# Kernel tuning notes

Measured on AMD Instinct MI355X. Metric: run time of the kernel, lower is better.

The kernel has to match this reference:

```python
import jax, jax.numpy as jnp
import numpy as np

B, L, D, NH = 4, 1500, 512, 8
HD = D // NH
EPS = 1e-8            # F.normalize eps
PEPS = 1.1920929e-07  # torch clamp_probs eps for float32
TEMP = 1.0


def setup_inputs():
    key = jax.random.key(0)
    ks = jax.random.split(key, 12)
    s = 1.0 / np.sqrt(D)
    eye = jnp.eye(D, dtype=jnp.float32)
    return {
        "hidden": jax.random.normal(ks[0], (B, L, D), jnp.float32),
        "lengths": jnp.ones((B,), jnp.float32),
        "u_noise": jax.random.uniform(ks[1], (B, L), jnp.float32),
        "W1": jax.random.normal(ks[2], (D, D), jnp.float32) * s,
        "b1": jnp.zeros((D,), jnp.float32),
        "W2": jax.random.normal(ks[3], (D, D), jnp.float32) * s,
        "b2": jnp.zeros((D,), jnp.float32),
        "Wq": eye + jax.random.normal(ks[4], (D, D), jnp.float32) * 0.01,
        "Wk": eye + jax.random.normal(ks[5], (D, D), jnp.float32) * 0.01,
        "sim_bias": jnp.float32(0.098),
        "learned_query": jax.random.normal(ks[6], (D,), jnp.float32),
        "Wpk": eye + jax.random.normal(ks[7], (D, D), jnp.float32) * 0.01,
        "Wpv": eye + jax.random.normal(ks[8], (D, D), jnp.float32) * 0.01,
        "Wpo": eye + jax.random.normal(ks[9], (D, D), jnp.float32) * 0.01,
        "ln_g": jnp.ones((D,), jnp.float32),
        "ln_b": jnp.zeros((D,), jnp.float32),
    }


def reference(hidden, lengths, u_noise, W1, b1, W2, b2, Wq, Wk, sim_bias,
              learned_query, Wpk, Wpv, Wpo, ln_g, ln_b):
    Bb, Ll, Dd = hidden.shape

    def nrm(x):
        n = jnp.sqrt(jnp.sum(x * x, -1, keepdims=True))
        return x / jnp.maximum(n, EPS)

    def mlp(x):
        return jax.nn.gelu(x @ W1.T + b1, approximate=False) @ W2.T + b2

    # boundary logits from adjacent-frame cosine similarity (dropout = eval identity)
    q_in = nrm(hidden[:, :-1]); q = nrm(mlp(q_in) + q_in) @ Wq.T
    k_in = nrm(hidden[:, 1:]);  k = nrm(mlp(k_in) + k_in) @ Wk.T
    cos = jnp.sum(q * k, -1)                                   # (B, L-1)
    probs = jnp.clip((1.0 - (cos + sim_bias)) * 0.5, 0.0, 1.0)
    probs = jnp.pad(probs, ((0, 0), (0, 1)))                   # (B, L)

    # RelaxedBernoulli rsample with explicit logistic noise
    p = jnp.clip(probs, PEPS, 1.0 - PEPS)
    u = jnp.clip(u_noise, PEPS, 1.0 - PEPS)
    soft = jax.nn.sigmoid((jnp.log(p) - jnp.log1p(-p) + jnp.log(u) - jnp.log1p(-u)) / TEMP)
    hard = (soft > 0.5).astype(hidden.dtype)

    idx = jnp.arange(Ll)
    valid_len = jnp.minimum((lengths * (Ll + 1)).astype(jnp.int32) - 1, Ll)
    trunc = (valid_len < Ll)[:, None]
    zmask = trunc & (idx[None] >= valid_len[:, None])
    omask = trunc & (idx[None] == valid_len[:, None])
    soft = jnp.where(omask, 1.0, jnp.where(zmask, 0.0, soft))
    hard = jnp.where(omask, 1.0, jnp.where(zmask, 0.0, hard))
    hard_b = hard - jax.lax.stop_gradient(soft) + soft         # straight-through
    # emergency boundary for all-zero rows
    no_b = (jnp.sum(hard, 1) == 0)[:, None]
    hard_b = jnp.where(no_b & (idx[None] == jnp.minimum(valid_len, Ll - 1)[:, None]), 1.0, hard_b)

    # segment membership (common()): token l in segment s iff exclusive cumsum == s
    seg = jnp.cumsum(hard_b, 1) - hard_b                       # (B, L)
    lmask = idx[None] < (lengths * Ll).astype(jnp.int32)[:, None]
    seg_mask = (seg[:, :, None] == idx[None, None, :].astype(hidden.dtype)) & lmask[:, :, None]  # (B,L,S)

    # layernorm + K/V projections
    mu = jnp.mean(hidden, -1, keepdims=True)
    hv = hidden - mu
    hn = hv / jnp.sqrt(jnp.mean(hv * hv, -1, keepdims=True) + 1e-5) * ln_g + ln_b
    keys = (hn @ Wpk.T).reshape(Bb, Ll, NH, HD)
    vals = (hn @ Wpv.T).reshape(Bb, Ll, NH, HD)

    # query is shared across segments -> scores only differ via the segment mask
    qh = learned_query.reshape(NH, HD)
    base = jnp.einsum('hd,blhd->bhl', qh, keys) * (HD ** -0.5)  # (B,H,L)
    mask_t = jnp.transpose(seg_mask, (0, 2, 1))[:, None]        # (B,1,S,L)
    sc = jnp.where(mask_t, base[:, :, None, :], -jnp.inf)       # (B,H,S,L)
    aw = jnp.nan_to_num(jax.nn.softmax(sc, axis=-1))            # empty segments -> 0 rows
    pooled = jnp.einsum('bhsl,blhd->bshd', aw, vals).reshape(Bb, Ll, Dd)
    return pooled @ Wpo.T                                       # (B, S=L, D)
```

## Files before the change

### kernel.cpp

```cpp
#include <hip/hip_runtime.h>
#include <math.h>

#define Bz 4
#define Lz 1500
#define Dz 512
#define NHz 8
#define Nz (Bz*Lz)
#define PEPSf 1.1920929e-07f

typedef __bf16 bf16x8 __attribute__((ext_vector_type(8)));
typedef unsigned short u16x8 __attribute__((ext_vector_type(8)));
typedef float f32x4 __attribute__((ext_vector_type(4)));
typedef unsigned short us;

__device__ __forceinline__ us f2bf(float f) {
  unsigned u = __float_as_uint(f);
  return (us)((u + 0x7fffu + ((u >> 16) & 1u)) >> 16);
}
__device__ __forceinline__ float bf2f(us b) {
  return __uint_as_float(((unsigned)b) << 16);
}
__device__ __forceinline__ int ti_idx(int row, int col) {
  return (((row >> 4) * 64 + (col >> 3)) << 7) + ((row & 15) << 3) + (col & 7);
}
__device__ __forceinline__ void st_tiled(us* __restrict__ P, int row, int col, us v) {
  P[ti_idx(row, col)] = v;
}

__device__ __forceinline__ bool decode_blk(int bx, int ncg, int& R, int& cg) {
  int xcd = bx & 7, v = bx >> 3;
  cg = v % ncg;
  R = (v / ncg) * 8 + xcd;
  return R < 94;
}

__global__ __launch_bounds__(256) void k_wconv(
    const float* __restrict__ s0, const float* __restrict__ s1, const float* __restrict__ s2,
    const float* __restrict__ s3,
    const float* __restrict__ Wq, const float* __restrict__ Wk,
    const float* __restrict__ Wpk, const float* __restrict__ lq,
    us* __restrict__ h0, us* __restrict__ h1, us* __restrict__ h2, us* __restrict__ h3,
    us* __restrict__ l0, us* __restrict__ l1,
    us* __restrict__ WkTh, us* __restrict__ WkTl, us* __restrict__ WqTh, us* __restrict__ WqTl,
    float* __restrict__ wqe) {
  const int rt = blockIdx.x, mat = blockIdx.y, t = threadIdx.x;
  if (mat == 8) {
    if (rt < 8) {
      for (int d = t; d < Dz; d += 256) {
        float acc = 0.f;
        for (int e = 0; e < 64; ++e) acc += lq[rt * 64 + e] * Wpk[(size_t)(rt * 64 + e) * Dz + d];
        wqe[rt * Dz + d] = acc;
      }
    }
    return;
  }
  const float* S; us* H; us* L = nullptr; bool tr = false;
  switch (mat) {
    case 0: S = s0; H = h0; L = l0; break;
    case 1: S = s1; H = h1; L = l1; break;
    case 2: S = s2; H = h2; break;
    case 3: S = s3; H = h3; break;
    case 4: S = Wk; H = WkTh; L = WkTl; tr = true; break;
    default: S = Wq; H = WqTh; L = WqTl; tr = true; break;
  }
  for (int e = t; e < 8192; e += 256) {
    int mm = e >> 9, c = e & 511;
    float x = tr ? S[(size_t)c * 512 + (rt * 16 + mm)]
                 : S[(size_t)(rt * 16 + mm) * 512 + c];
    us hb = f2bf(x);
    int off = ((rt * 64 + (c >> 3)) << 7) + (mm << 3) + (c & 7);
    H[off] = hb;
    if (L) L[off] = f2bf(x - bf2f(hb));
  }
}

__global__ __launch_bounds__(256) void k_rowprep(const float* __restrict__ h,
    const float* __restrict__ g, const float* __restrict__ bb,
    const float* __restrict__ wqe,
    us* __restrict__ Uh, us* __restrict__ Ul, us* __restrict__ HNh,
    float* __restrict__ base) {
  const int row = blockIdx.x;
  const int t = threadIdx.x;
  const float* x = h + (size_t)row * Dz;
  float x0 = x[t], x1 = x[t + 256];
  float s = x0 + x1, q = x0 * x0 + x1 * x1;
  #pragma unroll
  for (int o = 32; o > 0; o >>= 1) { s += __shfl_xor(s, o, 64); q += __shfl_xor(q, o, 64); }
  __shared__ float ls[4], lq[4];
  __shared__ float xs[Dz];
  if ((t & 63) == 0) { ls[t >> 6] = s; lq[t >> 6] = q; }
  __syncthreads();
  s = ls[0] + ls[1] + ls[2] + ls[3];
  q = lq[0] + lq[1] + lq[2] + lq[3];
  float un = 1.f / fmaxf(sqrtf(q), 1e-8f);
  float u0 = x0 * un, u1 = x1 * un;
  us hb0 = f2bf(u0), hb1 = f2bf(u1);
  st_tiled(Uh, row, t, hb0);       st_tiled(Ul, row, t, f2bf(u0 - bf2f(hb0)));
  st_tiled(Uh, row, t + 256, hb1); st_tiled(Ul, row, t + 256, f2bf(u1 - bf2f(hb1)));
  float mu = s * (1.f / 512.f);
  float var = fmaxf(q * (1.f / 512.f) - mu * mu, 0.f);
  float r = rsqrtf(var + 1e-5f);
  float hn0 = (x0 - mu) * r * g[t] + bb[t];
  float hn1 = (x1 - mu) * r * g[t + 256] + bb[t + 256];
  st_tiled(HNh, row, t, f2bf(hn0));
  st_tiled(HNh, row, t + 256, f2bf(hn1));
  xs[t] = hn0; xs[t + 256] = hn1;
  __syncthreads();
  const int hh = t >> 5, lane = t & 31;
  float accb = 0.f;
  for (int d = lane; d < Dz; d += 32) accb += xs[d] * wqe[hh * Dz + d];
  #pragma unroll
  for (int o = 16; o > 0; o >>= 1) accb += __shfl_xor(accb, o, 32);
  if (lane == 0) base[(size_t)row * NHz + hh] = accb * 0.125f;
}

template<int SPLIT>
__device__ __forceinline__ void gemm_body(
    const us* __restrict__ Ah, const us* __restrict__ Al,
    const us* __restrict__ Bh, const us* __restrict__ Bl,
    const float* __restrict__ bias,
    const us* __restrict__ addH, const us* __restrict__ addL, int doGelu,
    float* __restrict__ outF, us* __restrict__ outR,
    us* __restrict__ outH, us* __restrict__ outL,
    int R, int cg, int colbase, int Nrows) {
  const int t = threadIdx.x, w = t >> 6, l = t & 63;
  const int m = l & 15, q = l >> 4;
  const int wr = w & 1, wc = w >> 1;
  const int laneoff = q * 128 + m * 8;
  const int nrtm1 = (Nrows >> 4) - 1;

  const u16x8* pa[2]; const u16x8* pal[2];
  const u16x8* pb[2]; const u16x8* pbl[2];
  #pragma unroll
  for (int i = 0; i < 2; ++i) {
    int rt = min(R * 4 + wr * 2 + i, nrtm1);
    pa[i] = (const u16x8*)(Ah + (size_t)rt * 8192 + laneoff);
    if (SPLIT == 3) pal[i] = (const u16x8*)(Al + (size_t)rt * 8192 + laneoff);
  }
  #pragma unroll
  for (int j = 0; j < 2; ++j) {
    int ct = cg * 4 + wc * 2 + j;
    pb[j] = (const u16x8*)(Bh + (size_t)ct * 8192 + laneoff);
    if (SPLIT == 3) pbl[j] = (const u16x8*)(Bl + (size_t)ct * 8192 + laneoff);
  }

  u16x8 bAh[2][2], bAl[2][2], bBh[2][2], bBl[2][2];
  #pragma unroll
  for (int i = 0; i < 2; ++i) {
    bAh[0][i] = pa[i][0];
    if (SPLIT == 3) bAl[0][i] = pal[i][0];
  }
  #pragma unroll
  for (int j = 0; j < 2; ++j) {
    bBh[0][j] = pb[j][0];
    if (SPLIT == 3) bBl[0][j] = pbl[j][0];
  }

  f32x4 acc[2][2];
  #pragma unroll
  for (int i = 0; i < 2; ++i)
    #pragma unroll
    for (int j = 0; j < 2; ++j) acc[i][j] = (f32x4){0.f, 0.f, 0.f, 0.f};

  #pragma unroll 2
  for (int s = 0; s < 16; ++s) {
    const int cur = s & 1, nxt = cur ^ 1;
    const int sn = (s + 1) & 15;
    #pragma unroll
    for (int i = 0; i < 2; ++i) {
      bAh[nxt][i] = pa[i][sn * 64];
      if (SPLIT == 3) bAl[nxt][i] = pal[i][sn * 64];
    }
    #pragma unroll
    for (int j = 0; j < 2; ++j) {
      bBh[nxt][j] = pb[j][sn * 64];
      if (SPLIT == 3) bBl[nxt][j] = pbl[j][sn * 64];
    }
    #pragma unroll
    for (int i = 0; i < 2; ++i)
      #pragma unroll
      for (int j = 0; j < 2; ++j) {
        bf16x8 a = __builtin_bit_cast(bf16x8, bAh[cur][i]);
        bf16x8 b = __builtin_bit_cast(bf16x8, bBh[cur][j]);
        acc[i][j] = __builtin_amdgcn_mfma_f32_16x16x32_bf16(a, b, acc[i][j], 0, 0, 0);
        if (SPLIT == 3) {
          bf16x8 al_ = __builtin_bit_cast(bf16x8, bAl[cur][i]);
          bf16x8 bl_ = __builtin_bit_cast(bf16x8, bBl[cur][j]);
          acc[i][j] = __builtin_amdgcn_mfma_f32_16x16x32_bf16(a, bl_, acc[i][j], 0, 0, 0);
          acc[i][j] = __builtin_amdgcn_mfma_f32_16x16x32_bf16(al_, b, acc[i][j], 0, 0, 0);
        }
      }
  }

  const int row0 = R * 64 + wr * 32;
  const int col0 = colbase + wc * 32;
  #pragma unroll
  for (int i = 0; i < 2; ++i) {
    #pragma unroll
    for (int r = 0; r < 4; ++r) {
      const int grow = row0 + i * 16 + q * 4 + r;
      if (grow >= Nrows) continue;
      #pragma unroll
      for (int j = 0; j < 2; ++j) {
        const int gcol = col0 + j * 16 + m;
        float v = acc[i][j][r];
        if (bias)   v += bias[gcol];
        if (addH) {
          int ai = ti_idx(grow, gcol);
          v += bf2f(addH[ai]) + bf2f(addL[ai]);
        }
        if (doGelu) v = 0.5f * v * (1.f + erff(v * 0.70710678118654752f));
        if (outF) outF[(size_t)grow * Dz + gcol] = v;
        if (outR) outR[(size_t)grow * Dz + gcol] = f2bf(v);
        if (outH) {
          us hb = f2bf(v);
          st_tiled(outH, grow, gcol, hb);
          if (outL) st_tiled(outL, grow, gcol, f2bf(v - bf2f(hb)));
        }
      }
    }
  }
}

__global__ __launch_bounds__(256, 4) void g_t1_vals_gt(
    const us* Uh, const us* Ul, const us* W1h, const us* W1l, const float* b1, us* T1h, us* T1l,
    const us* HNh, const us* Wpvh, us* VALSb,
    const us* WkTh, const us* WkTl, const us* WqTh, const us* WqTl, us* Gth, us* Gtl) {
  if (blockIdx.z == 2) {
    int bx = blockIdx.x;
    if (bx >= 64) return;
    gemm_body<3>(WkTh, WkTl, WqTh, WqTl, nullptr, nullptr, nullptr, 0,
                 nullptr, nullptr, Gth, Gtl, bx >> 3, bx & 7, (bx & 7) * 64, 512);
    return;
  }
  int R, cg;
  if (!decode_blk(blockIdx.x, 8, R, cg)) return;
  if (blockIdx.z == 0)
    gemm_body<3>(Uh, Ul, W1h, W1l, b1, nullptr, nullptr, 1,
                 nullptr, nullptr, T1h, T1l, R, cg, cg * 64, Nz);
  else
    gemm_body<1>(HNh, nullptr, Wpvh, nullptr, nullptr, nullptr, nullptr, 0,
                 nullptr, VALSb, nullptr, nullptr, R, cg, cg * 64, Nz);
}

__global__ __launch_bounds__(256, 4) void g_w2(
    const us* T1h, const us* T1l, const us* W2h, const us* W2l, const float* b2,
    const us* Uh, const us* Ul, float* M, us* Mh, us* Ml) {
  int R, cg;
  if (!decode_blk(blockIdx.x, 8, R, cg)) return;
  gemm_body<3>(T1h, T1l, W2h, W2l, b2, Uh, Ul, 0, M, nullptr, Mh, Ml, R, cg, cg * 64, Nz);
}

__global__ __launch_bounds__(256, 4) void g_p(
    const us* Mh, const us* Ml, const us* Gth, const us* Gtl, float* P) {
  int R, cg;
  if (!decode_blk(blockIdx.x, 8, R, cg)) return;
  gemm_body<3>(Mh, Ml, Gth, Gtl, nullptr, nullptr, nullptr, 0,
               P, nullptr, nullptr, nullptr, R, cg, cg * 64, Nz);
}

__global__ __launch_bounds__(256, 4) void g_out(
    const us* Ph, const us* Wpoh, float* out) {
  int R, cg;
  if (!decode_blk(blockIdx.x, 8, R, cg)) return;
  gemm_body<1>(Ph, nullptr, Wpoh, nullptr, nullptr, nullptr, nullptr, 0,
               out, nullptr, nullptr, nullptr, R, cg, cg * 64, Nz);
}

__global__ __launch_bounds__(256) void k_probs(const float* __restrict__ P,
    const float* __restrict__ M, const float* __restrict__ simb,
    float* __restrict__ probs) {
  const int w = threadIdx.x >> 6, t = threadIdx.x & 63;
  const int l = blockIdx.x * 4 + w, b = blockIdx.y;
  if (l >= Lz) return;
  if (l == Lz - 1) { if (t == 0) probs[(size_t)b * Lz + l] = 0.f; return; }
  const float* pp = P + ((size_t)b * Lz + l) * Dz;
  const float* m0 = M + ((size_t)b * Lz + l) * Dz;
  const float* m1 = M + ((size_t)b * Lz + l + 1) * Dz;
  float accd = 0.f, q0 = 0.f, q1 = 0.f;
  for (int i = t; i < Dz; i += 64) {
    float a = pp[i], x0 = m0[i], x1 = m1[i];
    accd += a * x1; q0 += x0 * x0; q1 += x1 * x1;
  }
  #pragma unroll
  for (int o = 32; o > 0; o >>= 1) {
    accd += __shfl_xor(accd, o, 64);
    q0 += __shfl_xor(q0, o, 64);
    q1 += __shfl_xor(q1, o, 64);
  }
  if (t == 0) {
    float un0 = 1.f / fmaxf(sqrtf(q0), 1e-8f);
    float un1 = 1.f / fmaxf(sqrtf(q1), 1e-8f);
    float cosv = accd * un0 * un1;
    float p = (1.f - (cosv + simb[0])) * 0.5f;
    probs[(size_t)b * Lz + l] = fminf(fmaxf(p, 0.f), 1.f);
  }
}

__global__ __launch_bounds__(256) void k_boundary(const float* __restrict__ probs,
    const float* __restrict__ un, const float* __restrict__ lengths,
    int* __restrict__ seg_start, int* __restrict__ seg_meta) {
  const int b = blockIdx.x, t = threadIdx.x;
  __shared__ float hard[Lz];
  __shared__ float ps[256];
  __shared__ float ws4[4];
  const float len = lengths[b];
  const int valid_len = min((int)(len * (Lz + 1)) - 1, Lz);
  const int Lm = (int)(len * Lz);
  const bool trunc = valid_len < Lz;
  for (int l = t; l < Lz; l += 256) {
    float p = probs[(size_t)b * Lz + l];
    p = fminf(fmaxf(p, PEPSf), 1.f - PEPSf);
    float u = un[(size_t)b * Lz + l];
    u = fminf(fmaxf(u, PEPSf), 1.f - PEPSf);
    float z = logf(p) - log1pf(-p) + logf(u) - log1pf(-u);
    float soft = 1.f / (1.f + expf(-z));
    float hd = soft > 0.5f ? 1.f : 0.f;
    if (trunc && l >= valid_len) hd = (l == valid_len) ? 1.f : 0.f;
    hard[l] = hd;
  }
  __syncthreads();
  float sm = 0.f;
  for (int l = t; l < Lz; l += 256) sm += hard[l];
  #pragma unroll
  for (int o = 32; o > 0; o >>= 1) sm += __shfl_xor(sm, o, 64);
  if ((t & 63) == 0) ws4[t >> 6] = sm;
  __syncthreads();
  float total = ws4[0] + ws4[1] + ws4[2] + ws4[3];
  if (total == 0.f && t == 0) hard[min(valid_len, Lz - 1)] = 1.f;
  __syncthreads();
  const int l0 = t * 6;
  float loc = 0.f;
  for (int i = 0; i < 6; ++i) { int l = l0 + i; if (l < Lz) loc += hard[l]; }
  ps[t] = loc;
  __syncthreads();
  for (int off = 1; off < 256; off <<= 1) {
    float v = (t >= off) ? ps[t - off] : 0.f;
    __syncthreads();
    ps[t] += v;
    __syncthreads();
  }
  float run = ps[t] - loc;
  for (int i = 0; i < 6; ++i) {
    int l = l0 + i; if (l >= Lz) break;
    int seg = (int)(run + 0.5f);
    if (l == 0) seg_start[b * (Lz + 1) + 0] = 0;
    else if (hard[l - 1] > 0.5f) seg_start[b * (Lz + 1) + seg] = l;
    if (l == Lz - 1) {
      int nseg = seg + 1;
      seg_meta[b * 2 + 0] = nseg;
      seg_meta[b * 2 + 1] = Lm;
      seg_start[b * (Lz + 1) + nseg] = Lz;
    }
    run += hard[l];
  }
}

__global__ __launch_bounds__(256) void k_pool(const float* __restrict__ base,
    const us* __restrict__ VALSb, const int* __restrict__ seg_start,
    const int* __restrict__ seg_meta, us* __restrict__ Ph) {
  const int s = blockIdx.x, b = blockIdx.y, t = threadIdx.x;
  const int orow = b * Lz + s;
  const int nseg = seg_meta[b * 2], Lm = seg_meta[b * 2 + 1];
  int start = 0, end = 0;
  bool empty = true;
  if (s < nseg) {
    start = seg_start[b * (Lz + 1) + s];
    end = min(seg_start[b * (Lz + 1) + s + 1], Lm);
    empty = start >= end;
  }
  if (empty) { st_tiled(Ph, orow, t, 0); st_tiled(Ph, orow, t + 256, 0); return; }
  const int h = t >> 5, lane = t & 31;
  const float* bp = base + (size_t)b * Lz * NHz + h;
  float m = -1e30f;
  for (int l = start + lane; l < end; l += 32) m = fmaxf(m, bp[(size_t)l * NHz]);
  #pragma unroll
  for (int o = 16; o > 0; o >>= 1) m = fmaxf(m, __shfl_xor(m, o, 32));
  float den = 0.f;
  for (int l = start + lane; l < end; l += 32) den += expf(bp[(size_t)l * NHz] - m);
  #pragma unroll
  for (int o = 16; o > 0; o >>= 1) den += __shfl_xor(den, o, 32);
  float a0 = 0.f, a1 = 0.f;
  const us* vp = VALSb + (size_t)b * Lz * Dz + h * 64 + lane;
  for (int l = start; l < end; ++l) {
    float wgt = expf(bp[(size_t)l * NHz] - m);
    a0 += wgt * bf2f(vp[(size_t)l * Dz]);
    a1 += wgt * bf2f(vp[(size_t)l * Dz + 32]);
  }
  float inv = 1.f / den;
  st_tiled(Ph, orow, h * 64 + lane, f2bf(a0 * inv));
  st_tiled(Ph, orow, h * 64 + lane + 32, f2bf(a1 * inv));
}

extern "C" void kernel_launch(void* const* d_in, const int* in_sizes, int n_in,
                              void* d_out, int out_size, void* d_ws, size_t ws_size,
                              hipStream_t stream) {
  const float* hidden  = (const float*)d_in[0];
  const float* lengths = (const float*)d_in[1];
  const float* unoise  = (const float*)d_in[2];
  const float* W1  = (const float*)d_in[3];
  const float* b1  = (const float*)d_in[4];
  const float* W2  = (const float*)d_in[5];
  const float* b2  = (const float*)d_in[6];
  const float* Wq  = (const float*)d_in[7];
  const float* Wk  = (const float*)d_in[8];
  const float* simb   = (const float*)d_in[9];
  const float* lquery = (const float*)d_in[10];
  const float* Wpk = (const float*)d_in[11];
  const float* Wpv = (const float*)d_in[12];
  const float* Wpo = (const float*)d_in[13];
  const float* lng = (const float*)d_in[14];
  const float* lnb = (const float*)d_in[15];
  float* out = (float*)d_out;

  char* p = (char*)d_ws;
  const size_t SF = (size_t)Nz * Dz * 4;
  const size_t TP = (size_t)376 * 8192 * 2;
  const size_t WP = (size_t)32 * 8192 * 2;
  float* M    = (float*)p; p += SF;
  float* PF   = (float*)p; p += SF;
  us* VALSb = (us*)p; p += TP;
  us* Uh  = (us*)p; p += TP;
  us* Ul  = (us*)p; p += TP;
  us* T1h = (us*)p; p += TP;
  us* T1l = (us*)p; p += TP;
  us* Mh  = (us*)p; p += TP;
  us* Ml  = (us*)p; p += TP;
  us* HNh = (us*)p; p += TP;
  us* Ph  = (us*)p; p += TP;
  us* W1h = (us*)p; p += WP;
  us* W1l = (us*)p; p += WP;
  us* W2h = (us*)p; p += WP;
  us* W2l = (us*)p; p += WP;
  us* Wpvh = (us*)p; p += WP;
  us* Wpoh = (us*)p; p += WP;
  us* WkTh = (us*)p; p += WP;
  us* WkTl = (us*)p; p += WP;
  us* WqTh = (us*)p; p += WP;
  us* WqTl = (us*)p; p += WP;
  us* Gth  = (us*)p; p += WP;
  us* Gtl  = (us*)p; p += WP;
  float* probs  = (float*)p; p += 24064;
  float* base   = (float*)p; p += 192000;
  int* segst    = (int*)p;   p += 24064;
  int* segmeta  = (int*)p;   p += 256;
  float* wqe    = (float*)p;

  const int G8 = 8 * 12 * 8;

  k_wconv<<<dim3(32, 9), 256, 0, stream>>>(W1, W2, Wpv, Wpo, Wq, Wk, Wpk, lquery,
      W1h, W2h, Wpvh, Wpoh, W1l, W2l, WkTh, WkTl, WqTh, WqTl, wqe);
  k_rowprep<<<Nz, 256, 0, stream>>>(hidden, lng, lnb, wqe, Uh, Ul, HNh, base);
  g_t1_vals_gt<<<dim3(G8, 1, 3), 256, 0, stream>>>(Uh, Ul, W1h, W1l, b1, T1h, T1l,
      HNh, Wpvh, VALSb, WkTh, WkTl, WqTh, WqTl, Gth, Gtl);
  g_w2<<<G8, 256, 0, stream>>>(T1h, T1l, W2h, W2l, b2, Uh, Ul, M, Mh, Ml);
  g_p<<<G8, 256, 0, stream>>>(Mh, Ml, Gth, Gtl, PF);
  k_probs<<<dim3(375, Bz), 256, 0, stream>>>(PF, M, simb, probs);
  k_boundary<<<Bz, 256, 0, stream>>>(probs, unoise, lengths, segst, segmeta);
  k_pool<<<dim3(Lz, Bz), 256, 0, stream>>>(base, VALSb, segst, segmeta, Ph);
  g_out<<<G8, 256, 0, stream>>>(Ph, Wpoh, out);
}
```

Before: 234.9 us.

## Fuse cosine-similarity reductions into GEMM epilogues and drop k_probs kernel

Row norms of M are accumulated with atomics in the W2 GEMM epilogue, and the dot product of P with the next row of M is accumulated in the g_p epilogue, so the full fp32 P matrix is no longer written. The separate k_probs kernel is removed and k_boundary computes the probabilities from the accumulated norms and dots. This saves a 12 MB write and its re-read, plus one launch. In exchange it adds float atomics, which make the summation order nondeterministic, and extra scattered reads of M in the g_p epilogue.

```diff
diff --git a/kernel.cpp b/kernel.cpp
--- a/kernel.cpp
+++ b/kernel.cpp
@@ -78,9 +78,10 @@
     const float* __restrict__ g, const float* __restrict__ bb,
     const float* __restrict__ wqe,
     us* __restrict__ Uh, us* __restrict__ Ul, us* __restrict__ HNh,
-    float* __restrict__ base) {
+    float* __restrict__ base, float* __restrict__ nrmacc, float* __restrict__ dotacc) {
   const int row = blockIdx.x;
   const int t = threadIdx.x;
+  if (t == 0) { nrmacc[row] = 0.f; dotacc[row] = 0.f; }
   const float* x = h + (size_t)row * Dz;
   float x0 = x[t], x1 = x[t + 256];
   float s = x0 + x1, q = x0 * x0 + x1 * x1;
@@ -122,6 +123,7 @@
     const us* __restrict__ addH, const us* __restrict__ addL, int doGelu,
     float* __restrict__ outF, us* __restrict__ outR,
     us* __restrict__ outH, us* __restrict__ outL,
+    float* __restrict__ nrmAcc, float* __restrict__ dotAcc, const float* __restrict__ Mfull,
     int R, int cg, int colbase, int Nrows) {
   const int t = threadIdx.x, w = t >> 6, l = t & 63;
   const int m = l & 15, q = l >> 4;
@@ -200,6 +202,9 @@
     for (int r = 0; r < 4; ++r) {
       const int grow = row0 + i * 16 + q * 4 + r;
       if (grow >= Nrows) continue;
+      float pn = 0.f, pd = 0.f;
+      bool nd = false;
+      if (dotAcc) nd = ((grow % Lz) != (Lz - 1));
       #pragma unroll
       for (int j = 0; j < 2; ++j) {
         const int gcol = col0 + j * 16 + m;
@@ -217,6 +222,18 @@
           st_tiled(outH, grow, gcol, hb);
           if (outL) st_tiled(outL, grow, gcol, f2bf(v - bf2f(hb)));
         }
+        if (nrmAcc) pn += v * v;
+        if (dotAcc && nd) pd += v * Mfull[(size_t)(grow + 1) * Dz + gcol];
+      }
+      if (nrmAcc) {
+        #pragma unroll
+        for (int o = 8; o > 0; o >>= 1) pn += __shfl_xor(pn, o, 64);
+        if (m == 0) atomicAdd(nrmAcc + grow, pn);
+      }
+      if (dotAcc) {
+        #pragma unroll
+        for (int o = 8; o > 0; o >>= 1) pd += __shfl_xor(pd, o, 64);
+        if (m == 0 && nd) atomicAdd(dotAcc + grow, pd);
       }
     }
   }
@@ -230,33 +247,39 @@
     int bx = blockIdx.x;
     if (bx >= 64) return;
     gemm_body<3>(WkTh, WkTl, WqTh, WqTl, nullptr, nullptr, nullptr, 0,
-                 nullptr, nullptr, Gth, Gtl, bx >> 3, bx & 7, (bx & 7) * 64, 512);
+                 nullptr, nullptr, Gth, Gtl, nullptr, nullptr, nullptr,
+                 bx >> 3, bx & 7, (bx & 7) * 64, 512);
     return;
   }
   int R, cg;
   if (!decode_blk(blockIdx.x, 8, R, cg)) return;
   if (blockIdx.z == 0)
     gemm_body<3>(Uh, Ul, W1h, W1l, b1, nullptr, nullptr, 1,
-                 nullptr, nullptr, T1h, T1l, R, cg, cg * 64, Nz);
+                 nullptr, nullptr, T1h, T1l, nullptr, nullptr, nullptr,
+                 R, cg, cg * 64, Nz);
   else
     gemm_body<1>(HNh, nullptr, Wpvh, nullptr, nullptr, nullptr, nullptr, 0,
-                 nullptr, VALSb, nullptr, nullptr, R, cg, cg * 64, Nz);
+                 nullptr, VALSb, nullptr, nullptr, nullptr, nullptr, nullptr,
+                 R, cg, cg * 64, Nz);
 }
 
 __global__ __launch_bounds__(256, 4) void g_w2(
     const us* T1h, const us* T1l, const us* W2h, const us* W2l, const float* b2,
-    const us* Uh, const us* Ul, float* M, us* Mh, us* Ml) {
+    const us* Uh, const us* Ul, float* M, us* Mh, us* Ml, float* nrmacc) {
   int R, cg;
   if (!decode_blk(blockIdx.x, 8, R, cg)) return;
-  gemm_body<3>(T1h, T1l, W2h, W2l, b2, Uh, Ul, 0, M, nullptr, Mh, Ml, R, cg, cg * 64, Nz);
+  gemm_body<3>(T1h, T1l, W2h, W2l, b2, Uh, Ul, 0, M, nullptr, Mh, Ml,
+               nrmacc, nullptr, nullptr, R, cg, cg * 64, Nz);
 }
 
 __global__ __launch_bounds__(256, 4) void g_p(
-    const us* Mh, const us* Ml, const us* Gth, const us* Gtl, float* P) {
+    const us* Mh, const us* Ml, const us* Gth, const us* Gtl,
+    float* dotacc, const float* M) {
   int R, cg;
   if (!decode_blk(blockIdx.x, 8, R, cg)) return;
   gemm_body<3>(Mh, Ml, Gth, Gtl, nullptr, nullptr, nullptr, 0,
-               P, nullptr, nullptr, nullptr, R, cg, cg * 64, Nz);
+               nullptr, nullptr, nullptr, nullptr,
+               nullptr, dotacc, M, R, cg, cg * 64, Nz);
 }
 
 __global__ __launch_bounds__(256, 4) void g_out(
@@ -264,40 +287,12 @@
   int R, cg;
   if (!decode_blk(blockIdx.x, 8, R, cg)) return;
   gemm_body<1>(Ph, nullptr, Wpoh, nullptr, nullptr, nullptr, nullptr, 0,
-               out, nullptr, nullptr, nullptr, R, cg, cg * 64, Nz);
-}
-
-__global__ __launch_bounds__(256) void k_probs(const float* __restrict__ P,
-    const float* __restrict__ M, const float* __restrict__ simb,
-    float* __restrict__ probs) {
-  const int w = threadIdx.x >> 6, t = threadIdx.x & 63;
-  const int l = blockIdx.x * 4 + w, b = blockIdx.y;
-  if (l >= Lz) return;
-  if (l == Lz - 1) { if (t == 0) probs[(size_t)b * Lz + l] = 0.f; return; }
-  const float* pp = P + ((size_t)b * Lz + l) * Dz;
-  const float* m0 = M + ((size_t)b * Lz + l) * Dz;
-  const float* m1 = M + ((size_t)b * Lz + l + 1) * Dz;
-  float accd = 0.f, q0 = 0.f, q1 = 0.f;
-  for (int i = t; i < Dz; i += 64) {
-    float a = pp[i], x0 = m0[i], x1 = m1[i];
-    accd += a * x1; q0 += x0 * x0; q1 += x1 * x1;
-  }
-  #pragma unroll
-  for (int o = 32; o > 0; o >>= 1) {
-    accd += __shfl_xor(accd, o, 64);
-    q0 += __shfl_xor(q0, o, 64);
-    q1 += __shfl_xor(q1, o, 64);
-  }
-  if (t == 0) {
-    float un0 = 1.f / fmaxf(sqrtf(q0), 1e-8f);
-    float un1 = 1.f / fmaxf(sqrtf(q1), 1e-8f);
-    float cosv = accd * un0 * un1;
-    float p = (1.f - (cosv + simb[0])) * 0.5f;
-    probs[(size_t)b * Lz + l] = fminf(fmaxf(p, 0.f), 1.f);
-  }
-}
-
-__global__ __launch_bounds__(256) void k_boundary(const float* __restrict__ probs,
+               out, nullptr, nullptr, nullptr, nullptr, nullptr, nullptr,
+               R, cg, cg * 64, Nz);
+}
+
+__global__ __launch_bounds__(256) void k_boundary(const float* __restrict__ dotacc,
+    const float* __restrict__ nrmacc, const float* __restrict__ simb,
     const float* __restrict__ un, const float* __restrict__ lengths,
     int* __restrict__ seg_start, int* __restrict__ seg_meta) {
   const int b = blockIdx.x, t = threadIdx.x;
@@ -305,11 +300,23 @@
   __shared__ float ps[256];
   __shared__ float ws4[4];
   const float len = lengths[b];
+  const float sb = simb[0];
   const int valid_len = min((int)(len * (Lz + 1)) - 1, Lz);
   const int Lm = (int)(len * Lz);
   const bool trunc = valid_len < Lz;
   for (int l = t; l < Lz; l += 256) {
-    float p = probs[(size_t)b * Lz + l];
+    float p;
+    if (l == Lz - 1) {
+      p = 0.f;
+    } else {
+      float d  = dotacc[(size_t)b * Lz + l];
+      float n0 = nrmacc[(size_t)b * Lz + l];
+      float n1 = nrmacc[(size_t)b * Lz + l + 1];
+      float un0 = 1.f / fmaxf(sqrtf(n0), 1e-8f);
+      float un1 = 1.f / fmaxf(sqrtf(n1), 1e-8f);
+      float cosv = d * un0 * un1;
+      p = fminf(fmaxf((1.f - (cosv + sb)) * 0.5f, 0.f), 1.f);
+    }
     p = fminf(fmaxf(p, PEPSf), 1.f - PEPSf);
     float u = un[(size_t)b * Lz + l];
     u = fminf(fmaxf(u, PEPSf), 1.f - PEPSf);
@@ -418,7 +425,6 @@
   const size_t TP = (size_t)376 * 8192 * 2;
   const size_t WP = (size_t)32 * 8192 * 2;
   float* M    = (float*)p; p += SF;
-  float* PF   = (float*)p; p += SF;
   us* VALSb = (us*)p; p += TP;
   us* Uh  = (us*)p; p += TP;
   us* Ul  = (us*)p; p += TP;
@@ -440,7 +446,8 @@
   us* WqTl = (us*)p; p += WP;
   us* Gth  = (us*)p; p += WP;
   us* Gtl  = (us*)p; p += WP;
-  float* probs  = (float*)p; p += 24064;
+  float* dotacc = (float*)p; p += 24064;
+  float* nrmacc = (float*)p; p += 24064;
   float* base   = (float*)p; p += 192000;
   int* segst    = (int*)p;   p += 24064;
   int* segmeta  = (int*)p;   p += 256;
@@ -450,13 +457,12 @@
 
   k_wconv<<<dim3(32, 9), 256, 0, stream>>>(W1, W2, Wpv, Wpo, Wq, Wk, Wpk, lquery,
       W1h, W2h, Wpvh, Wpoh, W1l, W2l, WkTh, WkTl, WqTh, WqTl, wqe);
-  k_rowprep<<<Nz, 256, 0, stream>>>(hidden, lng, lnb, wqe, Uh, Ul, HNh, base);
+  k_rowprep<<<Nz, 256, 0, stream>>>(hidden, lng, lnb, wqe, Uh, Ul, HNh, base, nrmacc, dotacc);
   g_t1_vals_gt<<<dim3(G8, 1, 3), 256, 0, stream>>>(Uh, Ul, W1h, W1l, b1, T1h, T1l,
       HNh, Wpvh, VALSb, WkTh, WkTl, WqTh, WqTl, Gth, Gtl);
-  g_w2<<<G8, 256, 0, stream>>>(T1h, T1l, W2h, W2l, b2, Uh, Ul, M, Mh, Ml);
-  g_p<<<G8, 256, 0, stream>>>(Mh, Ml, Gth, Gtl, PF);
-  k_probs<<<dim3(375, Bz), 256, 0, stream>>>(PF, M, simb, probs);
-  k_boundary<<<Bz, 256, 0, stream>>>(probs, unoise, lengths, segst, segmeta);
+  g_w2<<<G8, 256, 0, stream>>>(T1h, T1l, W2h, W2l, b2, Uh, Ul, M, Mh, Ml, nrmacc);
+  g_p<<<G8, 256, 0, stream>>>(Mh, Ml, Gth, Gtl, dotacc, M);
+  k_boundary<<<Bz, 256, 0, stream>>>(dotacc, nrmacc, simb, unoise, lengths, segst, segmeta);
   k_pool<<<dim3(Lz, Bz), 256, 0, stream>>>(base, VALSb, segst, segmeta, Ph);
   g_out<<<G8, 256, 0, stream>>>(Ph, Wpoh, out);
 }
```

Measured after the change: 240.2 us. 1.02x slower.

## Merge weight conversion with row prep and move base dot into phase-2 GEMM launch

Applied to the files above, without the earlier changes.

Combines weight conversion and per-row normalization/layernorm into one launch, which removes the dependency of row prep on wqe. The per-row head-score dot with wqe moves into the phase-2 GEMM launch as extra blocks that read hi/lo-split layernorm output. This needs a new HNl buffer and extra tiled writes. The segment-boundary prefix sum now uses wave shuffles instead of a shared-memory scan with many barriers. Together these cut kernel launches and serialization, at the cost of writing and reading more layernorm data.

```diff
diff --git a/kernel.cpp b/kernel.cpp
--- a/kernel.cpp
+++ b/kernel.cpp
@@ -34,7 +34,9 @@
   return R < 94;
 }
 
-__global__ __launch_bounds__(256) void k_wconv(
+__global__ __launch_bounds__(256) void k_prep(
+    const float* __restrict__ hidden,
+    const float* __restrict__ g, const float* __restrict__ bb,
     const float* __restrict__ s0, const float* __restrict__ s1, const float* __restrict__ s2,
     const float* __restrict__ s3,
     const float* __restrict__ Wq, const float* __restrict__ Wk,
@@ -42,56 +44,53 @@
     us* __restrict__ h0, us* __restrict__ h1, us* __restrict__ h2, us* __restrict__ h3,
     us* __restrict__ l0, us* __restrict__ l1,
     us* __restrict__ WkTh, us* __restrict__ WkTl, us* __restrict__ WqTh, us* __restrict__ WqTl,
-    float* __restrict__ wqe) {
-  const int rt = blockIdx.x, mat = blockIdx.y, t = threadIdx.x;
-  if (mat == 8) {
-    if (rt < 8) {
-      for (int d = t; d < Dz; d += 256) {
-        float acc = 0.f;
-        for (int e = 0; e < 64; ++e) acc += lq[rt * 64 + e] * Wpk[(size_t)(rt * 64 + e) * Dz + d];
-        wqe[rt * Dz + d] = acc;
+    float* __restrict__ wqe,
+    us* __restrict__ Uh, us* __restrict__ Ul, us* __restrict__ HNh, us* __restrict__ HNl) {
+  const int t = threadIdx.x;
+  if (blockIdx.x < 288) {
+    const int u = blockIdx.x, rt = u & 31, mat = u >> 5;
+    if (mat == 8) {
+      if (rt < 8) {
+        for (int d = t; d < Dz; d += 256) {
+          float acc = 0.f;
+          for (int e = 0; e < 64; ++e)
+            acc += lq[rt * 64 + e] * Wpk[(size_t)(rt * 64 + e) * Dz + d];
+          wqe[rt * Dz + d] = acc;
+        }
       }
+      return;
+    }
+    const float* S; us* H; us* L = nullptr; bool tr = false;
+    switch (mat) {
+      case 0: S = s0; H = h0; L = l0; break;
+      case 1: S = s1; H = h1; L = l1; break;
+      case 2: S = s2; H = h2; break;
+      case 3: S = s3; H = h3; break;
+      case 4: S = Wk; H = WkTh; L = WkTl; tr = true; break;
+      default: S = Wq; H = WqTh; L = WqTl; tr = true; break;
+    }
+    for (int e = t; e < 8192; e += 256) {
+      int mm = e >> 9, c = e & 511;
+      float x = tr ? S[(size_t)c * 512 + (rt * 16 + mm)]
+                   : S[(size_t)(rt * 16 + mm) * 512 + c];
+      us hb = f2bf(x);
+      int off = ((rt * 64 + (c >> 3)) << 7) + (mm << 3) + (c & 7);
+      H[off] = hb;
+      if (L) L[off] = f2bf(x - bf2f(hb));
     }
     return;
   }
-  const float* S; us* H; us* L = nullptr; bool tr = false;
-  switch (mat) {
-    case 0: S = s0; H = h0; L = l0; break;
-    case 1: S = s1; H = h1; L = l1; break;
-    case 2: S = s2; H = h2; break;
-    case 3: S = s3; H = h3; break;
-    case 4: S = Wk; H = WkTh; L = WkTl; tr = true; break;
-    default: S = Wq; H = WqTh; L = WqTl; tr = true; break;
-  }
-  for (int e = t; e < 8192; e += 256) {
-    int mm = e >> 9, c = e & 511;
-    float x = tr ? S[(size_t)c * 512 + (rt * 16 + mm)]
-                 : S[(size_t)(rt * 16 + mm) * 512 + c];
-    us hb = f2bf(x);
-    int off = ((rt * 64 + (c >> 3)) << 7) + (mm << 3) + (c & 7);
-    H[off] = hb;
-    if (L) L[off] = f2bf(x - bf2f(hb));
-  }
-}
-
-__global__ __launch_bounds__(256) void k_rowprep(const float* __restrict__ h,
-    const float* __restrict__ g, const float* __restrict__ bb,
-    const float* __restrict__ wqe,
-    us* __restrict__ Uh, us* __restrict__ Ul, us* __restrict__ HNh,
-    float* __restrict__ base) {
-  const int row = blockIdx.x;
-  const int t = threadIdx.x;
-  const float* x = h + (size_t)row * Dz;
+  const int row = blockIdx.x - 288;
+  const float* x = hidden + (size_t)row * Dz;
   float x0 = x[t], x1 = x[t + 256];
   float s = x0 + x1, q = x0 * x0 + x1 * x1;
   #pragma unroll
   for (int o = 32; o > 0; o >>= 1) { s += __shfl_xor(s, o, 64); q += __shfl_xor(q, o, 64); }
-  __shared__ float ls[4], lq[4];
-  __shared__ float xs[Dz];
-  if ((t & 63) == 0) { ls[t >> 6] = s; lq[t >> 6] = q; }
+  __shared__ float ls[4], lqs[4];
+  if ((t & 63) == 0) { ls[t >> 6] = s; lqs[t >> 6] = q; }
   __syncthreads();
   s = ls[0] + ls[1] + ls[2] + ls[3];
-  q = lq[0] + lq[1] + lq[2] + lq[3];
+  q = lqs[0] + lqs[1] + lqs[2] + lqs[3];
   float un = 1.f / fmaxf(sqrtf(q), 1e-8f);
   float u0 = x0 * un, u1 = x1 * un;
   us hb0 = f2bf(u0), hb1 = f2bf(u1);
@@ -102,16 +101,9 @@
   float r = rsqrtf(var + 1e-5f);
   float hn0 = (x0 - mu) * r * g[t] + bb[t];
   float hn1 = (x1 - mu) * r * g[t + 256] + bb[t + 256];
-  st_tiled(HNh, row, t, f2bf(hn0));
-  st_tiled(HNh, row, t + 256, f2bf(hn1));
-  xs[t] = hn0; xs[t + 256] = hn1;
-  __syncthreads();
-  const int hh = t >> 5, lane = t & 31;
-  float accb = 0.f;
-  for (int d = lane; d < Dz; d += 32) accb += xs[d] * wqe[hh * Dz + d];
-  #pragma unroll
-  for (int o = 16; o > 0; o >>= 1) accb += __shfl_xor(accb, o, 32);
-  if (lane == 0) base[(size_t)row * NHz + hh] = accb * 0.125f;
+  us nb0 = f2bf(hn0), nb1 = f2bf(hn1);
+  st_tiled(HNh, row, t, nb0);       st_tiled(HNl, row, t, f2bf(hn0 - bf2f(nb0)));
+  st_tiled(HNh, row, t + 256, nb1); st_tiled(HNl, row, t + 256, f2bf(hn1 - bf2f(nb1)));
 }
 
 template<int SPLIT>
@@ -222,25 +214,52 @@
   }
 }
 
-__global__ __launch_bounds__(256, 4) void g_t1_vals_gt(
+__global__ __launch_bounds__(256, 4) void g_phase2(
     const us* Uh, const us* Ul, const us* W1h, const us* W1l, const float* b1, us* T1h, us* T1l,
-    const us* HNh, const us* Wpvh, us* VALSb,
-    const us* WkTh, const us* WkTl, const us* WqTh, const us* WqTl, us* Gth, us* Gtl) {
-  if (blockIdx.z == 2) {
-    int bx = blockIdx.x;
-    if (bx >= 64) return;
+    const us* HNh, const us* HNl, const us* Wpvh, us* VALSb,
+    const us* WkTh, const us* WkTl, const us* WqTh, const us* WqTl, us* Gth, us* Gtl,
+    const float* wqe, float* base) {
+  const int u = blockIdx.x;
+  if (u < 768) {
+    int R, c;
+    if (decode_blk(u, 8, R, c))
+      gemm_body<3>(Uh, Ul, W1h, W1l, b1, nullptr, nullptr, 1,
+                   nullptr, nullptr, T1h, T1l, R, c, c * 64, Nz);
+    return;
+  }
+  if (u < 1536) {
+    int R, c;
+    if (decode_blk(u - 768, 8, R, c))
+      gemm_body<1>(HNh, nullptr, Wpvh, nullptr, nullptr, nullptr, nullptr, 0,
+                   nullptr, VALSb, nullptr, nullptr, R, c, c * 64, Nz);
+    return;
+  }
+  if (u < 1600) {
+    int bx = u - 1536;
     gemm_body<3>(WkTh, WkTl, WqTh, WqTl, nullptr, nullptr, nullptr, 0,
                  nullptr, nullptr, Gth, Gtl, bx >> 3, bx & 7, (bx & 7) * 64, 512);
     return;
   }
-  int R, cg;
-  if (!decode_blk(blockIdx.x, 8, R, cg)) return;
-  if (blockIdx.z == 0)
-    gemm_body<3>(Uh, Ul, W1h, W1l, b1, nullptr, nullptr, 1,
-                 nullptr, nullptr, T1h, T1l, R, cg, cg * 64, Nz);
-  else
-    gemm_body<1>(HNh, nullptr, Wpvh, nullptr, nullptr, nullptr, nullptr, 0,
-                 nullptr, VALSb, nullptr, nullptr, R, cg, cg * 64, Nz);
+  const int u94 = u - 1600, t = threadIdx.x;
+  #pragma unroll
+  for (int pp = 0; pp < 2; ++pp) {
+    const int p = t + pp * 256;
+    const int row = u94 * 64 + (p >> 3), h = p & 7;
+    if (row >= Nz) continue;
+    const float* wq = wqe + h * Dz;
+    const int rb = ((row >> 4) * 64) << 7;
+    const int ro = (row & 15) << 3;
+    float acc = 0.f;
+    for (int c8 = 0; c8 < 64; ++c8) {
+      const int off = rb + (c8 << 7) + ro;
+      u16x8 hv = *(const u16x8*)(HNh + off);
+      u16x8 lv = *(const u16x8*)(HNl + off);
+      #pragma unroll
+      for (int k = 0; k < 8; ++k)
+        acc += (bf2f(hv[k]) + bf2f(lv[k])) * wq[c8 * 8 + k];
+    }
+    base[(size_t)row * NHz + h] = acc * 0.125f;
+  }
 }
 
 __global__ __launch_bounds__(256, 4) void g_w2(
@@ -302,8 +321,8 @@
     int* __restrict__ seg_start, int* __restrict__ seg_meta) {
   const int b = blockIdx.x, t = threadIdx.x;
   __shared__ float hard[Lz];
-  __shared__ float ps[256];
   __shared__ float ws4[4];
+  __shared__ float wsum[4];
   const float len = lengths[b];
   const int valid_len = min((int)(len * (Lz + 1)) - 1, Lz);
   const int Lm = (int)(len * Lz);
@@ -332,15 +351,18 @@
   const int l0 = t * 6;
   float loc = 0.f;
   for (int i = 0; i < 6; ++i) { int l = l0 + i; if (l < Lz) loc += hard[l]; }
-  ps[t] = loc;
+  const int wid = t >> 6, lane = t & 63;
+  float v = loc;
+  #pragma unroll
+  for (int o = 1; o < 64; o <<= 1) {
+    float n = __shfl_up(v, o, 64);
+    if (lane >= o) v += n;
+  }
+  if (lane == 63) wsum[wid] = v;
   __syncthreads();
-  for (int off = 1; off < 256; off <<= 1) {
-    float v = (t >= off) ? ps[t - off] : 0.f;
-    __syncthreads();
-    ps[t] += v;
-    __syncthreads();
-  }
-  float run = ps[t] - loc;
+  float woff = 0.f;
+  for (int ww = 0; ww < wid; ++ww) woff += wsum[ww];
+  float run = v + woff - loc;
   for (int i = 0; i < 6; ++i) {
     int l = l0 + i; if (l >= Lz) break;
     int seg = (int)(run + 0.5f);
@@ -427,6 +449,7 @@
   us* Mh  = (us*)p; p += TP;
   us* Ml  = (us*)p; p += TP;
   us* HNh = (us*)p; p += TP;
+  us* HNl = (us*)p; p += TP;
   us* Ph  = (us*)p; p += TP;
   us* W1h = (us*)p; p += WP;
   us* W1l = (us*)p; p += WP;
@@ -448,11 +471,11 @@
 
   const int G8 = 8 * 12 * 8;
 
-  k_wconv<<<dim3(32, 9), 256, 0, stream>>>(W1, W2, Wpv, Wpo, Wq, Wk, Wpk, lquery,
-      W1h, W2h, Wpvh, Wpoh, W1l, W2l, WkTh, WkTl, WqTh, WqTl, wqe);
-  k_rowprep<<<Nz, 256, 0, stream>>>(hidden, lng, lnb, wqe, Uh, Ul, HNh, base);
-  g_t1_vals_gt<<<dim3(G8, 1, 3), 256, 0, stream>>>(Uh, Ul, W1h, W1l, b1, T1h, T1l,
-      HNh, Wpvh, VALSb, WkTh, WkTl, WqTh, WqTl, Gth, Gtl);
+  k_prep<<<288 + Nz, 256, 0, stream>>>(hidden, lng, lnb, W1, W2, Wpv, Wpo, Wq, Wk,
+      Wpk, lquery, W1h, W2h, Wpvh, Wpoh, W1l, W2l, WkTh, WkTl, WqTh, WqTl, wqe,
+      Uh, Ul, HNh, HNl);
+  g_phase2<<<1694, 256, 0, stream>>>(Uh, Ul, W1h, W1l, b1, T1h, T1l,
+      HNh, HNl, Wpvh, VALSb, WkTh, WkTl, WqTh, WqTl, Gth, Gtl, wqe, base);
   g_w2<<<G8, 256, 0, stream>>>(T1h, T1l, W2h, W2l, b2, Uh, Ul, M, Mh, Ml);
   g_p<<<G8, 256, 0, stream>>>(Mh, Ml, Gth, Gtl, PF);
   k_probs<<<dim3(375, Bz), 256, 0, stream>>>(PF, M, simb, probs);
```

Result: slower. 250.0 us (+6.4%).
